# Optimization experiments

Hardware: AMD Instinct MI355X
Metric: run time of the kernel (lower is better)

Reference implementation:

```python
import jax, jax.numpy as jnp
import numpy as np

N, E = 50000, 250000          # nodes, edges
IN, OUT, EDIM = 9, 84, 1      # NNConv(9, 84), edge nn Linear(1, 9*84)
EPS = 1e-5                    # BatchNorm1d default eps


def setup_inputs() -> dict:
    key = jax.random.key(0)
    ks = jax.random.split(key, 8)
    return {
        "x": jax.random.normal(ks[0], (N, IN), jnp.float32),
        "edge_index": jax.random.randint(ks[1], (2, E), 0, N, dtype=jnp.int64),
        "edge_attr": jax.random.normal(ks[2], (E, EDIM), jnp.float32),
        # edge nn: Linear(EDIM, IN*OUT) generating per-edge weight matrices
        "nn_w": jax.random.normal(ks[3], (EDIM, IN * OUT), jnp.float32) * (1.0 / np.sqrt(EDIM)),
        "nn_b": jnp.zeros((IN * OUT,), jnp.float32),
        # NNConv root weight + bias
        "root": jax.random.normal(ks[4], (IN, OUT), jnp.float32) * (1.0 / np.sqrt(IN)),
        "bias": jnp.zeros((OUT,), jnp.float32),
        # BatchNorm1d(84) affine params
        "gamma": jnp.ones((OUT,), jnp.float32),
        "beta": jnp.zeros((OUT,), jnp.float32),
    }


def reference(x, edge_index, edge_attr, nn_w, nn_b, root, bias, gamma, beta):
    src, dst = edge_index[0], edge_index[1]
    # per-edge weight matrices: [E, IN, OUT]
    w_e = (edge_attr @ nn_w + nn_b).reshape(E, IN, OUT)
    # gather source node features and apply edge-specific matmul: [E, OUT]
    msg = jnp.einsum('ei,eio->eo', x[src], w_e)
    # scatter-add to destination nodes (NNConv default aggr='add'): [N, OUT]
    aggr = jax.ops.segment_sum(msg, dst, num_segments=N)
    out = x @ root + aggr + bias
    # BatchNorm1d(84), training mode (biased batch stats)
    mean = out.mean(0)
    var = out.var(0)
    out = (out - mean) * jax.lax.rsqrt(var + EPS) * gamma + beta
    return out
```

## Files before the change

kernel.cpp:

```cpp
#include <hip/hip_runtime.h>

#define N_NODES 50000
#define E_EDGES 250000
#define IN_F 9
#define OUT_F 84
#define GROUPS 21
#define BN_EPS 1e-5f

#define NB_TILE 48
#define NTILES ((N_NODES + NB_TILE - 1) / NB_TILE)
#define NCOPIES 32
#define CAP 32

#define VDIM 27
#define NPAIR 378
#define NM 405
#define SLEN 408
#define VSTR 52
#define NSLOT 196

#define FB_TILE 96
#define FB_NT ((N_NODES + FB_TILE - 1) / FB_TILE)
#define VTS 28

#define CNT_OFF   0
#define STATC_OFF 50048
#define ZERO_WORDS 63104
#define SLOT_OFF  63232
#define S_OFF     3263232
#define SS_OFF    4163232

__global__ __launch_bounds__(256)
void fill_slots_kernel(const int* __restrict__ ei,
                       const float* __restrict__ ea,
                       int* __restrict__ cnt,
                       int2* __restrict__ slot) {
    int e = (blockIdx.x * blockDim.x + threadIdx.x) * 4;
    if (e < E_EDGES) {
        int4   s4 = *(const int4*)&ei[e];
        int4   d4 = *(const int4*)&ei[E_EDGES + e];
        float4 a4 = *(const float4*)&ea[e];
        int pos;
        pos = atomicAdd(&cnt[d4.x], 1);
        if (pos < CAP) slot[d4.x * CAP + pos] = make_int2(s4.x, __float_as_int(a4.x));
        pos = atomicAdd(&cnt[d4.y], 1);
        if (pos < CAP) slot[d4.y * CAP + pos] = make_int2(s4.y, __float_as_int(a4.y));
        pos = atomicAdd(&cnt[d4.z], 1);
        if (pos < CAP) slot[d4.z * CAP + pos] = make_int2(s4.z, __float_as_int(a4.z));
        pos = atomicAdd(&cnt[d4.w], 1);
        if (pos < CAP) slot[d4.w * CAP + pos] = make_int2(s4.w, __float_as_int(a4.w));
    }
}

__global__ void gather_gram_kernel(const float* __restrict__ x,
                                   const int*   __restrict__ cnt,
                                   const int2*  __restrict__ slot,
                                   float* __restrict__ S,
                                   float* __restrict__ statc) {
    __shared__ __align__(16) float V[VDIM * VSTR];
    __shared__ __align__(16) int2 rec[NB_TILE][CAP];
    __shared__ int cnt_s[NB_TILE];
    __shared__ unsigned char sI[NSLOT], sJ[NSLOT];

    const int tid = threadIdx.x;
    const int nbase = blockIdx.x * NB_TILE;

    for (int t = tid; t < NSLOT; t += blockDim.x) {
        int tt = t, i = 0;
        while (tt >= ((VDIM - i + 1) >> 1)) { tt -= (VDIM - i + 1) >> 1; ++i; }
        sI[t] = (unsigned char)i;
        sJ[t] = (unsigned char)(i + 2 * tt);
    }
    for (int t = tid; t < VDIM * 4; t += blockDim.x)
        V[(t >> 2) * VSTR + NB_TILE + (t & 3)] = 0.f;
    if (tid < NB_TILE) {
        int n = nbase + tid;
        int c = (n < N_NODES) ? cnt[n] : 0;
        cnt_s[tid] = (c > CAP) ? CAP : c;
    }
    __syncthreads();

    if (tid < NB_TILE * 4) {
        int nl = tid >> 2, part = tid & 3;
        int c = cnt_s[nl];
        const int4* grow = (const int4*)&slot[(nbase + nl) * CAP];
        int4* lrow = (int4*)&rec[nl][0];
#pragma unroll
        for (int j = 0; j < 4; ++j) {
            int s = part * 8 + j * 2;
            if (s < c) lrow[part * 4 + j] = grow[part * 4 + j];
        }
    }
    __syncthreads();

    for (int it = tid; it < NB_TILE * IN_F; it += blockDim.x) {
        int nl = it / IN_F, i = it - nl * IN_F;
        int n = nbase + nl;
        float xv = 0.f, s0 = 0.f, s1 = 0.f;
        if (n < N_NODES) {
            xv = x[n * IN_F + i];
            int c = cnt_s[nl];
            const int2* r = rec[nl];
            int k = 0;
            for (; k + 4 <= c; k += 4) {
                int2 r0 = r[k], r1 = r[k+1], r2 = r[k+2], r3 = r[k+3];
                float a0 = x[r0.x * IN_F + i];
                float a1 = x[r1.x * IN_F + i];
                float a2 = x[r2.x * IN_F + i];
                float a3 = x[r3.x * IN_F + i];
                s0 += (a0 + a1) + (a2 + a3);
                s1 += __int_as_float(r0.y) * a0 + __int_as_float(r1.y) * a1
                    + __int_as_float(r2.y) * a2 + __int_as_float(r3.y) * a3;
            }
            for (; k < c; ++k) {
                int2 r0 = r[k];
                float a0 = x[r0.x * IN_F + i];
                s0 += a0;
                s1 += __int_as_float(r0.y) * a0;
            }
            S[n * 18 + i]     = s0;
            S[n * 18 + 9 + i] = s1;
        }
        V[i * VSTR + nl]        = xv;
        V[(9 + i) * VSTR + nl]  = s0;
        V[(18 + i) * VSTR + nl] = s1;
    }
    __syncthreads();

    float* sc = statc + (blockIdx.x & (NCOPIES - 1)) * SLEN;
    for (int t = tid; t < NSLOT + VDIM; t += blockDim.x) {
        if (t < NSLOT) {
            int i = sI[t], j0 = sJ[t];
            int h2 = (j0 < VDIM - 1);
            const float4* vi = (const float4*)&V[i * VSTR];
            const float4* va = (const float4*)&V[j0 * VSTR];
            const float4* vb = (const float4*)&V[(j0 + h2) * VSTR];
            float acc0 = 0.f, acc1 = 0.f;
#pragma unroll
            for (int m = 0; m < VSTR / 4; ++m) {
                float4 a = vi[m], p = va[m], q = vb[m];
                acc0 += a.x * p.x + a.y * p.y + a.z * p.z + a.w * p.w;
                acc1 += a.x * q.x + a.y * q.y + a.z * q.z + a.w * q.w;
            }
            int base = i * VDIM - (i * (i - 1)) / 2;
            atomicAdd(&sc[base + (j0 - i)], acc0);
            if (h2) atomicAdd(&sc[base + (j0 - i) + 1], acc1);
        } else {
            int r = t - NSLOT;
            const float4* vi = (const float4*)&V[r * VSTR];
            float acc = 0.f;
#pragma unroll
            for (int m = 0; m < VSTR / 4; ++m) {
                float4 a = vi[m];
                acc += (a.x + a.y) + (a.z + a.w);
            }
            atomicAdd(&sc[NPAIR + r], acc);
        }
    }
}

__global__ __launch_bounds__(256)
void scale_kernel(const float* __restrict__ nw,
                  const float* __restrict__ nb,
                  const float* __restrict__ root,
                  const float* __restrict__ bias,
                  const float* __restrict__ gamma,
                  const float* __restrict__ beta,
                  const float* __restrict__ statc,
                  float* __restrict__ ss) {
    __shared__ float M[NM];
    const int tid = threadIdx.x;
    for (int t = tid; t < NM; t += blockDim.x) {
        float a = 0.f;
#pragma unroll
        for (int c = 0; c < NCOPIES; ++c) a += statc[c * SLEN + t];
        M[t] = a;
    }
    __syncthreads();
    if (tid < OUT_F) {
        const int o = tid;
        float c[VDIM];
#pragma unroll
        for (int i = 0; i < IN_F; ++i) {
            c[i]      = root[i * OUT_F + o];
            c[9 + i]  = nb[i * OUT_F + o];
            c[18 + i] = nw[i * OUT_F + o];
        }
        float sv = 0.f;
#pragma unroll
        for (int i = 0; i < VDIM; ++i) sv += M[NPAIR + i] * c[i];
        float q = 0.f;
        int t2 = 0;
        for (int i = 0; i < VDIM; ++i) {
            q += c[i] * c[i] * M[t2++];
            for (int j = i + 1; j < VDIM; ++j)
                q += 2.f * c[i] * c[j] * M[t2++];
        }
        const float b = bias[o];
        const float inv_n = 1.0f / (float)N_NODES;
        float mean  = (sv + (float)N_NODES * b) * inv_n;
        float sumsq = q + 2.f * b * sv + (float)N_NODES * b * b;
        float var   = sumsq * inv_n - mean * mean;
        float scl   = rsqrtf(var + BN_EPS) * gamma[o];
        ss[o]         = scl;
        ss[OUT_F + o] = beta[o] - mean * scl;
    }
}

__global__ __launch_bounds__(256, 2)
void final_kernel(const float* __restrict__ x,
                  const float* __restrict__ S,
                  const float* __restrict__ nw,
                  const float* __restrict__ nb,
                  const float* __restrict__ root,
                  const float* __restrict__ bias,
                  const float* __restrict__ ss,
                  float* __restrict__ out) {
    __shared__ __align__(16) float4 Ws[IN_F * GROUPS];
    __shared__ __align__(16) float4 Bs[IN_F * GROUPS];
    __shared__ __align__(16) float4 Rs[IN_F * GROUPS];
    __shared__ __align__(16) float Vt[FB_TILE * VTS];

    const int tid = threadIdx.x;
    const int nbase = blockIdx.x * FB_TILE;
    const int nn = (N_NODES - nbase < FB_TILE) ? (N_NODES - nbase) : FB_TILE;

    for (int t = tid; t < IN_F * GROUPS; t += blockDim.x) {
        Ws[t] = ((const float4*)nw)[t];
        Bs[t] = ((const float4*)nb)[t];
        Rs[t] = ((const float4*)root)[t];
    }

    {
        const float4* xs = (const float4*)(x + nbase * IN_F);
        const int nf4 = (nn * IN_F) >> 2;
        for (int f = tid; f < nf4; f += blockDim.x) {
            float4 v = xs[f];
            int fl = f * 4;
            int nl0 = fl / 9,       i0 = fl - nl0 * 9;
            int nl1 = (fl + 1) / 9, i1 = (fl + 1) - nl1 * 9;
            int nl2 = (fl + 2) / 9, i2 = (fl + 2) - nl2 * 9;
            int nl3 = (fl + 3) / 9, i3 = (fl + 3) - nl3 * 9;
            Vt[nl0 * VTS + i0] = v.x;
            Vt[nl1 * VTS + i1] = v.y;
            Vt[nl2 * VTS + i2] = v.z;
            Vt[nl3 * VTS + i3] = v.w;
        }
    }
    {
        const float4* s4 = (const float4*)(S + nbase * 18);
        const int nf4 = (nn * 18) >> 2;
        for (int f = tid; f < nf4; f += blockDim.x) {
            float4 v = s4[f];
            int fl = f * 4;
            int nl0 = fl / 18,       j0 = fl - nl0 * 18;
            int nl1 = (fl + 1) / 18, j1 = (fl + 1) - nl1 * 18;
            int nl2 = (fl + 2) / 18, j2 = (fl + 2) - nl2 * 18;
            int nl3 = (fl + 3) / 18, j3 = (fl + 3) - nl3 * 18;
            Vt[nl0 * VTS + 9 + j0] = v.x;
            Vt[nl1 * VTS + 9 + j1] = v.y;
            Vt[nl2 * VTS + 9 + j2] = v.z;
            Vt[nl3 * VTS + 9 + j3] = v.w;
        }
    }
    __syncthreads();

    const int g = tid % GROUPS;
    const int lane = tid / GROUPS;
    if (tid < 252) {
        float4 C[27];
#pragma unroll
        for (int i = 0; i < IN_F; ++i) {
            C[i]      = Rs[i * GROUPS + g];
            C[9 + i]  = Bs[i * GROUPS + g];
            C[18 + i] = Ws[i * GROUPS + g];
        }
        const float4 b4  = ((const float4*)bias)[g];
        const float4 sc4 = ((const float4*)ss)[g];
        const float4 sh4 = ((const float4*)(ss + OUT_F))[g];
#pragma unroll
        for (int k = 0; k < 8; ++k) {
            const int nl = k * 12 + lane;
            const int n  = nbase + nl;
            if (n < N_NODES) {
                const float* vr = &Vt[nl * VTS];
                float4 a0 = *(const float4*)(vr + 0);
                float4 a1 = *(const float4*)(vr + 4);
                float4 a2 = *(const float4*)(vr + 8);
                float4 a3 = *(const float4*)(vr + 12);
                float4 a4 = *(const float4*)(vr + 16);
                float4 a5 = *(const float4*)(vr + 20);
                float4 a6 = *(const float4*)(vr + 24);
                float4 acc = b4;
#define ACC(VC, IDX)                                                      \
                acc.x += (VC) * C[IDX].x;                                 \
                acc.y += (VC) * C[IDX].y;                                 \
                acc.z += (VC) * C[IDX].z;                                 \
                acc.w += (VC) * C[IDX].w;
                ACC(a0.x, 0)  ACC(a0.y, 1)  ACC(a0.z, 2)  ACC(a0.w, 3)
                ACC(a1.x, 4)  ACC(a1.y, 5)  ACC(a1.z, 6)  ACC(a1.w, 7)
                ACC(a2.x, 8)  ACC(a2.y, 9)  ACC(a2.z, 10) ACC(a2.w, 11)
                ACC(a3.x, 12) ACC(a3.y, 13) ACC(a3.z, 14) ACC(a3.w, 15)
                ACC(a4.x, 16) ACC(a4.y, 17) ACC(a4.z, 18) ACC(a4.w, 19)
                ACC(a5.x, 20) ACC(a5.y, 21) ACC(a5.z, 22) ACC(a5.w, 23)
                ACC(a6.x, 24) ACC(a6.y, 25) ACC(a6.z, 26)
#undef ACC
                acc.x = acc.x * sc4.x + sh4.x;
                acc.y = acc.y * sc4.y + sh4.y;
                acc.z = acc.z * sc4.z + sh4.z;
                acc.w = acc.w * sc4.w + sh4.w;
                *(float4*)&out[n * OUT_F + g * 4] = acc;
            }
        }
    }
}

extern "C" void kernel_launch(void* const* d_in, const int* in_sizes, int n_in,
                              void* d_out, int out_size, void* d_ws, size_t ws_size,
                              hipStream_t stream) {
    const float* x     = (const float*)d_in[0];
    const int*   ei    = (const int*)d_in[1];
    const float* ea    = (const float*)d_in[2];
    const float* nw    = (const float*)d_in[3];
    const float* nb    = (const float*)d_in[4];
    const float* root  = (const float*)d_in[5];
    const float* bias  = (const float*)d_in[6];
    const float* gamma = (const float*)d_in[7];
    const float* beta  = (const float*)d_in[8];
    float*       out   = (float*)d_out;

    float* wsf   = (float*)d_ws;
    int*   wsi   = (int*)d_ws;
    int*   cnt   = wsi + CNT_OFF;
    float* statc = wsf + STATC_OFF;
    int2*  slot  = (int2*)(wsi + SLOT_OFF);
    float* S     = wsf + S_OFF;
    float* ss    = wsf + SS_OFF;

    hipMemsetAsync(wsi, 0, ZERO_WORDS * sizeof(int), stream);
    fill_slots_kernel<<<(E_EDGES / 4 + 255) / 256, 256, 0, stream>>>(ei, ea, cnt, slot);
    gather_gram_kernel<<<NTILES, 256, 0, stream>>>(x, cnt, slot, S, statc);
    scale_kernel<<<1, 256, 0, stream>>>(nw, nb, root, bias, gamma, beta, statc, ss);
    final_kernel<<<FB_NT, 256, 0, stream>>>(x, S, nw, nb, root, bias, ss, out);
}
```

Before: 116.5 us.

## Pad x to 12-float rows and gather edges per-edge with LDS atomics

The fill kernel gains extra blocks that copy x into a 16-byte-aligned padded layout (12 floats per node) and zero the stat buffer, which shrinks the memset. The gather kernel compacts a tile's edge records into one flat list. Each thread then handles one edge, loading the source row with vector loads and accumulating into shared-memory sums with LDS float atomics. This replaces the old per-(node,feature) loop that did scalar gathers with uneven per-node work. The cost is extra traffic to write xp and contention on the shared atomics.

```diff
diff --git a/kernel.cpp b/kernel.cpp
--- a/kernel.cpp
+++ b/kernel.cpp
@@ -18,49 +18,78 @@
 #define SLEN 408
 #define VSTR 52
 #define NSLOT 196
+#define MAXEDG (NB_TILE * CAP)
+#define SASTR 19
 
 #define FB_TILE 96
 #define FB_NT ((N_NODES + FB_TILE - 1) / FB_TILE)
 #define VTS 28
 
+#define EB ((E_EDGES / 4 + 255) / 256)
+#define XB ((N_NODES + 255) / 256)
+
 #define CNT_OFF   0
 #define STATC_OFF 50048
-#define ZERO_WORDS 63104
+#define ZERO_WORDS 50000
 #define SLOT_OFF  63232
 #define S_OFF     3263232
 #define SS_OFF    4163232
+#define XP_OFF    4163400
 
 __global__ __launch_bounds__(256)
 void fill_slots_kernel(const int* __restrict__ ei,
                        const float* __restrict__ ea,
+                       const float* __restrict__ x,
                        int* __restrict__ cnt,
-                       int2* __restrict__ slot) {
-    int e = (blockIdx.x * blockDim.x + threadIdx.x) * 4;
-    if (e < E_EDGES) {
-        int4   s4 = *(const int4*)&ei[e];
-        int4   d4 = *(const int4*)&ei[E_EDGES + e];
-        float4 a4 = *(const float4*)&ea[e];
-        int pos;
-        pos = atomicAdd(&cnt[d4.x], 1);
-        if (pos < CAP) slot[d4.x * CAP + pos] = make_int2(s4.x, __float_as_int(a4.x));
-        pos = atomicAdd(&cnt[d4.y], 1);
-        if (pos < CAP) slot[d4.y * CAP + pos] = make_int2(s4.y, __float_as_int(a4.y));
-        pos = atomicAdd(&cnt[d4.z], 1);
-        if (pos < CAP) slot[d4.z * CAP + pos] = make_int2(s4.z, __float_as_int(a4.z));
-        pos = atomicAdd(&cnt[d4.w], 1);
-        if (pos < CAP) slot[d4.w * CAP + pos] = make_int2(s4.w, __float_as_int(a4.w));
-    }
-}
-
-__global__ void gather_gram_kernel(const float* __restrict__ x,
+                       int2* __restrict__ slot,
+                       float* __restrict__ xp,
+                       float* __restrict__ statc) {
+    const int bx = blockIdx.x, tid = threadIdx.x;
+    if (bx < EB) {
+        int e = (bx * 256 + tid) * 4;
+        if (e < E_EDGES) {
+            int4   s4 = *(const int4*)&ei[e];
+            int4   d4 = *(const int4*)&ei[E_EDGES + e];
+            float4 a4 = *(const float4*)&ea[e];
+            int pos;
+            pos = atomicAdd(&cnt[d4.x], 1);
+            if (pos < CAP) slot[d4.x * CAP + pos] = make_int2(s4.x, __float_as_int(a4.x));
+            pos = atomicAdd(&cnt[d4.y], 1);
+            if (pos < CAP) slot[d4.y * CAP + pos] = make_int2(s4.y, __float_as_int(a4.y));
+            pos = atomicAdd(&cnt[d4.z], 1);
+            if (pos < CAP) slot[d4.z * CAP + pos] = make_int2(s4.z, __float_as_int(a4.z));
+            pos = atomicAdd(&cnt[d4.w], 1);
+            if (pos < CAP) slot[d4.w * CAP + pos] = make_int2(s4.w, __float_as_int(a4.w));
+        }
+    } else {
+        if (bx == EB) {
+            float4* sc4 = (float4*)statc;
+            for (int t = tid; t < 13056 / 4; t += 256)
+                sc4[t] = make_float4(0.f, 0.f, 0.f, 0.f);
+        }
+        int n = (bx - EB) * 256 + tid;
+        if (n < N_NODES) {
+            const float* xr = x + n * IN_F;
+            float4* xd = (float4*)&xp[n * 12];
+            xd[0] = make_float4(xr[0], xr[1], xr[2], xr[3]);
+            xd[1] = make_float4(xr[4], xr[5], xr[6], xr[7]);
+            xd[2] = make_float4(xr[8], 0.f, 0.f, 0.f);
+        }
+    }
+}
+
+__global__ void gather_gram_kernel(const float* __restrict__ xp,
                                    const int*   __restrict__ cnt,
                                    const int2*  __restrict__ slot,
                                    float* __restrict__ S,
                                    float* __restrict__ statc) {
     __shared__ __align__(16) float V[VDIM * VSTR];
-    __shared__ __align__(16) int2 rec[NB_TILE][CAP];
+    __shared__ __align__(16) int2 lrec[MAXEDG];
+    __shared__ unsigned char lnl[MAXEDG];
+    __shared__ __align__(16) float Sacc[2 * NB_TILE * SASTR];
     __shared__ int cnt_s[NB_TILE];
     __shared__ unsigned char sI[NSLOT], sJ[NSLOT];
+    __shared__ int nedge;
 
     const int tid = threadIdx.x;
     const int nbase = blockIdx.x * NB_TILE;
@@ -73,23 +102,61 @@
     }
     for (int t = tid; t < VDIM * 4; t += blockDim.x)
         V[(t >> 2) * VSTR + NB_TILE + (t & 3)] = 0.f;
+    {
+        float4* sa4 = (float4*)Sacc;
+        for (int t = tid; t < (2 * NB_TILE * SASTR) / 4; t += blockDim.x)
+            sa4[t] = make_float4(0.f, 0.f, 0.f, 0.f);
+    }
     if (tid < NB_TILE) {
         int n = nbase + tid;
         int c = (n < N_NODES) ? cnt[n] : 0;
         cnt_s[tid] = (c > CAP) ? CAP : c;
     }
+    if (tid == 0) nedge = 0;
     __syncthreads();
 
     if (tid < NB_TILE * 4) {
         int nl = tid >> 2, part = tid & 3;
         int c = cnt_s[nl];
-        const int4* grow = (const int4*)&slot[(nbase + nl) * CAP];
-        int4* lrow = (int4*)&rec[nl][0];
-#pragma unroll
-        for (int j = 0; j < 4; ++j) {
-            int s = part * 8 + j * 2;
-            if (s < c) lrow[part * 4 + j] = grow[part * 4 + j];
-        }
+        int sbase = part * 8;
+        int nv = c - sbase;
+        nv = (nv < 0) ? 0 : ((nv > 8) ? 8 : nv);
+        if (nv > 0) {
+            const int4* grow = (const int4*)&slot[(nbase + nl) * CAP + sbase];
+            int4 q0 = grow[0], q1 = grow[1], q2 = grow[2], q3 = grow[3];
+            int pos = atomicAdd(&nedge, nv);
+            unsigned char nlc = (unsigned char)nl;
+#define APP(P, HI, LO)                                                   \
+            if ((P) < nv) { lrec[pos + (P)] = make_int2(HI, LO);         \
+                            lnl[pos + (P)] = nlc; }
+            APP(0, q0.x, q0.y) APP(1, q0.z, q0.w)
+            APP(2, q1.x, q1.y) APP(3, q1.z, q1.w)
+            APP(4, q2.x, q2.y) APP(5, q2.z, q2.w)
+            APP(6, q3.x, q3.y) APP(7, q3.z, q3.w)
+#undef APP
+        }
+    }
+    __syncthreads();
+
+    const int ne = nedge;
+    for (int t = tid; t < ne; t += blockDim.x) {
+        int2 r = lrec[t];
+        int nl = lnl[t];
+        float w = __int_as_float(r.y);
+        const float4* xr = (const float4*)&xp[r.x * 12];
+        float4 a = xr[0], b = xr[1];
+        float  c8 = xr[2].x;
+        float* s0 = &Sacc[nl * SASTR];
+        float* s1 = &Sacc[NB_TILE * SASTR + nl * SASTR];
+        atomicAdd(&s0[0], a.x);  atomicAdd(&s1[0], w * a.x);
+        atomicAdd(&s0[1], a.y);  atomicAdd(&s1[1], w * a.y);
+        atomicAdd(&s0[2], a.z);  atomicAdd(&s1[2], w * a.z);
+        atomicAdd(&s0[3], a.w);  atomicAdd(&s1[3], w * a.w);
+        atomicAdd(&s0[4], b.x);  atomicAdd(&s1[4], w * b.x);
+        atomicAdd(&s0[5], b.y);  atomicAdd(&s1[5], w * b.y);
+        atomicAdd(&s0[6], b.z);  atomicAdd(&s1[6], w * b.z);
+        atomicAdd(&s0[7], b.w);  atomicAdd(&s1[7], w * b.w);
+        atomicAdd(&s0[8], c8);   atomicAdd(&s1[8], w * c8);
     }
     __syncthreads();
 
@@ -98,26 +165,9 @@
         int n = nbase + nl;
         float xv = 0.f, s0 = 0.f, s1 = 0.f;
         if (n < N_NODES) {
-            xv = x[n * IN_F + i];
-            int c = cnt_s[nl];
-            const int2* r = rec[nl];
-            int k = 0;
-            for (; k + 4 <= c; k += 4) {
-                int2 r0 = r[k], r1 = r[k+1], r2 = r[k+2], r3 = r[k+3];
-                float a0 = x[r0.x * IN_F + i];
-                float a1 = x[r1.x * IN_F + i];
-                float a2 = x[r2.x * IN_F + i];
-                float a3 = x[r3.x * IN_F + i];
-                s0 += (a0 + a1) + (a2 + a3);
-                s1 += __int_as_float(r0.y) * a0 + __int_as_float(r1.y) * a1
-                    + __int_as_float(r2.y) * a2 + __int_as_float(r3.y) * a3;
-            }
-            for (; k < c; ++k) {
-                int2 r0 = r[k];
-                float a0 = x[r0.x * IN_F + i];
-                s0 += a0;
-                s1 += __int_as_float(r0.y) * a0;
-            }
+            xv = xp[n * 12 + i];
+            s0 = Sacc[nl * SASTR + i];
+            s1 = Sacc[NB_TILE * SASTR + nl * SASTR + i];
             S[n * 18 + i]     = s0;
             S[n * 18 + 9 + i] = s1;
         }
@@ -336,10 +386,11 @@
     int2*  slot  = (int2*)(wsi + SLOT_OFF);
     float* S     = wsf + S_OFF;
     float* ss    = wsf + SS_OFF;
+    float* xp    = wsf + XP_OFF;
 
     hipMemsetAsync(wsi, 0, ZERO_WORDS * sizeof(int), stream);
-    fill_slots_kernel<<<(E_EDGES / 4 + 255) / 256, 256, 0, stream>>>(ei, ea, cnt, slot);
-    gather_gram_kernel<<<NTILES, 256, 0, stream>>>(x, cnt, slot, S, statc);
+    fill_slots_kernel<<<EB + XB, 256, 0, stream>>>(ei, ea, x, cnt, slot, xp, statc);
+    gather_gram_kernel<<<NTILES, 256, 0, stream>>>(xp, cnt, slot, S, statc);
     scale_kernel<<<1, 256, 0, stream>>>(nw, nb, root, bias, gamma, beta, statc, ss);
     final_kernel<<<FB_NT, 256, 0, stream>>>(x, S, nw, nb, root, bias, ss, out);
 }
```

New measurement: 147.7 us. 1.27x slower.
